# Kernel tuning notes

Hardware: AMD Instinct MI355X
Metric: run time of the kernel (lower is better)

The kernel has to match this reference:

```python
import jax, jax.numpy as jnp
import numpy as np

N = 50000      # nodes of type 'student'
E = 625000     # edges per relation
H = 128        # hidden_channels
C = 6          # num_classes
F_IN = 3       # hardcoded num_features in the module


def setup_inputs() -> dict:
    key = jax.random.key(0)
    ks = jax.random.split(key, 32)
    s = 0.05
    d = {}
    d["x_student"] = jax.random.normal(ks[0], (N, F_IN), dtype=jnp.float32)
    d["ei_friend"] = jax.random.randint(ks[1], (2, E), 0, N)
    d["ei_study"] = jax.random.randint(ks[2], (2, E), 0, N)
    # embedding Linear(3 -> H)
    d["emb_w"] = jax.random.normal(ks[3], (F_IN, H), dtype=jnp.float32) * s
    d["emb_b"] = jnp.zeros((H,), jnp.float32)
    # per-layer, per-edge-type RGCNConv params: relation-0 weight, root weight, bias
    i = 4
    for l in range(2):
        for e in ("f", "s"):
            d[f"w_rel_{l}_{e}"] = jax.random.normal(ks[i], (H, H), dtype=jnp.float32) * s; i += 1
            d[f"w_root_{l}_{e}"] = jax.random.normal(ks[i], (H, H), dtype=jnp.float32) * s; i += 1
            d[f"b_{l}_{e}"] = jnp.zeros((H,), jnp.float32)
    # output Linear(H -> C)
    d["out_w"] = jax.random.normal(ks[i], (H, C), dtype=jnp.float32) * s
    d["out_b"] = jnp.zeros((C,), jnp.float32)
    return d


def _rgcn_conv(h, ei, w_rel, w_root, b):
    # PyG RGCNConv with edge_type==0 everywhere: mean-aggregate src features at dst,
    # project by relation-0 weight, add root transform and bias.
    src, dst = ei[0], ei[1]
    msg = h[src]                                             # [E, H] gather
    agg = jax.ops.segment_sum(msg, dst, num_segments=N)      # [N, H]
    deg = jax.ops.segment_sum(jnp.ones((ei.shape[1],), h.dtype), dst, num_segments=N)
    agg = agg / jnp.maximum(deg, 1.0)[:, None]               # mean aggr (0 for isolated nodes)
    return agg @ w_rel + h @ w_root + b


def reference(x_student, ei_friend, ei_study, emb_w, emb_b,
              w_rel_0_f, w_root_0_f, b_0_f, w_rel_0_s, w_root_0_s, b_0_s,
              w_rel_1_f, w_root_1_f, b_1_f, w_rel_1_s, w_root_1_s, b_1_s,
              out_w, out_b):
    h = jax.nn.relu(x_student @ emb_w + emb_b)
    # layer 0: sum over the two relations, divide by valid_edge_count=2, relu (dropout eval=no-op)
    acc = _rgcn_conv(h, ei_friend, w_rel_0_f, w_root_0_f, b_0_f) \
        + _rgcn_conv(h, ei_study, w_rel_0_s, w_root_0_s, b_0_s)
    h = jax.nn.relu(acc / 2.0)
    # layer 1 (last): no relu/dropout
    acc = _rgcn_conv(h, ei_friend, w_rel_1_f, w_root_1_f, b_1_f) \
        + _rgcn_conv(h, ei_study, w_rel_1_s, w_root_1_s, b_1_s)
    h = acc / 2.0
    return h @ out_w + out_b
```

## Files before the change

kernel.cpp:

```cpp
#include <hip/hip_runtime.h>

#define NN 50000
#define NE 625000
#define HD 128
#define CAP 40
#define ZROW NN

typedef __attribute__((ext_vector_type(8))) short short8;
typedef __attribute__((ext_vector_type(4))) float f32x4;
typedef __attribute__((ext_vector_type(4))) unsigned uint4v;

__device__ __forceinline__ unsigned short f2bf(float f) {
    unsigned u = __builtin_bit_cast(unsigned, f);
    u += 0x7FFFu + ((u >> 16) & 1u);
    return (unsigned short)(u >> 16);
}
__device__ __forceinline__ float bflo(unsigned v) { unsigned u = v << 16; return __builtin_bit_cast(float, u); }
__device__ __forceinline__ float bfhi(unsigned v) { unsigned u = v & 0xFFFF0000u; return __builtin_bit_cast(float, u); }

__device__ __forceinline__ void extract8(uint4v u, int j0, int cnt, unsigned* out) {
    unsigned raw[8];
    raw[0] = u.x & 0xFFFFu; raw[1] = u.x >> 16;
    raw[2] = u.y & 0xFFFFu; raw[3] = u.y >> 16;
    raw[4] = u.z & 0xFFFFu; raw[5] = u.z >> 16;
    raw[6] = u.w & 0xFFFFu; raw[7] = u.w >> 16;
    #pragma unroll
    for (int j = 0; j < 8; ++j) out[j] = (j0 + j < cnt) ? raw[j] : ZROW;
}

__global__ __launch_bounds__(256) void k_prep(
    const float* __restrict__ x, const float* __restrict__ w,
    const float* __restrict__ b, unsigned* __restrict__ h0, unsigned* __restrict__ h1,
    const int* __restrict__ ei_f, const int* __restrict__ ei_s,
    int* __restrict__ degF, int* __restrict__ degS,
    unsigned short* __restrict__ bktF, unsigned short* __restrict__ bktS,
    const float* __restrict__ wrf0, const float* __restrict__ wtf0, const float* __restrict__ bf0,
    const float* __restrict__ wrs0, const float* __restrict__ wts0, const float* __restrict__ bs0,
    const float* __restrict__ wrf1, const float* __restrict__ wtf1, const float* __restrict__ bf1,
    const float* __restrict__ wrs1, const float* __restrict__ wts1, const float* __restrict__ bs1,
    unsigned short* __restrict__ Wt, float* __restrict__ bcat)
{
    int bid = blockIdx.x, t = threadIdx.x;
    if (bid < 12500) {
        int i = bid * 256 + t;
        int n = i >> 6, c = (i & 63) * 2;
        float x0 = x[n*3+0], x1 = x[n*3+1], x2 = x[n*3+2];
        float v0 = fmaf(x0, w[c],   fmaf(x1, w[HD+c],   fmaf(x2, w[2*HD+c],   b[c])));
        float v1 = fmaf(x0, w[c+1], fmaf(x1, w[HD+c+1], fmaf(x2, w[2*HD+c+1], b[c+1])));
        v0 = fmaxf(v0, 0.f); v1 = fmaxf(v1, 0.f);
        h0[i] = (unsigned)f2bf(v0) | ((unsigned)f2bf(v1) << 16);
    } else if (bid == 12500) {
        if (t < 64)       h0[(long)ZROW*64 + t] = 0u;
        else if (t < 128) h1[(long)ZROW*64 + (t - 64)] = 0u;
    } else if (bid < 12885) {
        int i = (bid - 12501) * 256 + t;
        int ln = i / 384, k = i - ln * 384;
        int l = ln >> 7, n = ln & 127;
        const float* wrf = l ? wrf1 : wrf0;
        const float* wrs = l ? wrs1 : wrs0;
        const float* wtf = l ? wtf1 : wtf0;
        const float* wts = l ? wts1 : wts0;
        float v;
        if (k < 128)      v = wrf[k*HD + n];
        else if (k < 256) v = wrs[(k-128)*HD + n];
        else              v = wtf[(k-256)*HD + n] + wts[(k-256)*HD + n];
        Wt[(long)ln*384 + k] = f2bf(0.5f * v);
        if (i < 256) {
            int ll = i >> 7, cc = i & 127;
            const float* bfp = ll ? bf1 : bf0;
            const float* bsp = ll ? bs1 : bs0;
            bcat[i] = 0.5f * (bfp[cc] + bsp[cc]);
        }
    } else {
        int bq = bid - 12885;
        int rel = bq >= 1960;
        int bqq = bq - rel * 1960;
        int cls = bqq & 7;
        int chunk = bqq >> 3;
        const int* ei; int* deg; unsigned short* bkt;
        if (rel == 0) { ei = ei_f; deg = degF; bkt = bktF; }
        else          { ei = ei_s; deg = degS; bkt = bktS; }
        const int lo = cls * 6250, hi = lo + 6250;
        int e0 = chunk * 2560 + t;
        #pragma unroll
        for (int i = 0; i < 10; ++i) {
            int e = e0 + i * 256;
            if (e >= NE) continue;
            int d = ei[NE + e];
            if (d >= lo && d < hi) {
                int s = ei[e];
                int pos = atomicAdd(&deg[d], 1);
                if (pos < CAP) bkt[d*CAP + pos] = (unsigned short)s;
            }
        }
    }
}

__global__ __launch_bounds__(256) void k_spmm(
    const unsigned* __restrict__ h,
    const int* __restrict__ degF, const int* __restrict__ degS,
    const unsigned short* __restrict__ bktF, const unsigned short* __restrict__ bktS,
    unsigned* __restrict__ aggF, unsigned* __restrict__ aggS)
{
    int w = threadIdx.x >> 6, lane = threadIdx.x & 63;
    int n = blockIdx.x * 4 + w;
    int dF = degF[n], dS = degS[n];
    int cF = min(dF, CAP), cS = min(dS, CAP);
    const unsigned short* rowF = bktF + n*CAP;
    const unsigned short* rowS = bktS + n*CAP;
    uint4v uF0 = *(const uint4v*)(rowF);
    uint4v uF1 = *(const uint4v*)(rowF + 8);
    uint4v uS0 = *(const uint4v*)(rowS);
    uint4v uS1 = *(const uint4v*)(rowS + 8);
    unsigned iF[16], iS[16];
    extract8(uF0, 0, cF, iF); extract8(uF1, 8, cF, iF + 8);
    extract8(uS0, 0, cS, iS); extract8(uS1, 8, cS, iS + 8);
    unsigned vF[16], vS[16];
    #pragma unroll
    for (int j = 0; j < 16; ++j) vF[j] = h[iF[j]*64u + lane];
    #pragma unroll
    for (int j = 0; j < 16; ++j) vS[j] = h[iS[j]*64u + lane];
    float aF0 = 0.f, aF1 = 0.f, aS0 = 0.f, aS1 = 0.f;
    #pragma unroll
    for (int j = 0; j < 16; ++j) { aF0 += bflo(vF[j]); aF1 += bfhi(vF[j]); }
    #pragma unroll
    for (int j = 0; j < 16; ++j) { aS0 += bflo(vS[j]); aS1 += bfhi(vS[j]); }
    for (int j = 16; j < cF; j += 8) {
        uint4v u = *(const uint4v*)(rowF + j);
        unsigned ii[8];
        extract8(u, j, cF, ii);
        unsigned vv[8];
        #pragma unroll
        for (int q = 0; q < 8; ++q) vv[q] = h[ii[q]*64u + lane];
        #pragma unroll
        for (int q = 0; q < 8; ++q) { aF0 += bflo(vv[q]); aF1 += bfhi(vv[q]); }
    }
    for (int j = 16; j < cS; j += 8) {
        uint4v u = *(const uint4v*)(rowS + j);
        unsigned ii[8];
        extract8(u, j, cS, ii);
        unsigned vv[8];
        #pragma unroll
        for (int q = 0; q < 8; ++q) vv[q] = h[ii[q]*64u + lane];
        #pragma unroll
        for (int q = 0; q < 8; ++q) { aS0 += bflo(vv[q]); aS1 += bfhi(vv[q]); }
    }
    float invF = 1.f / fmaxf((float)dF, 1.f);
    float invS = 1.f / fmaxf((float)dS, 1.f);
    aggF[n*64 + lane] = (unsigned)f2bf(aF0*invF) | ((unsigned)f2bf(aF1*invF) << 16);
    aggS[n*64 + lane] = (unsigned)f2bf(aS0*invS) | ((unsigned)f2bf(aS1*invS) << 16);
}

__global__ __launch_bounds__(256) void k_gemm(
    const unsigned short* __restrict__ A0, const unsigned short* __restrict__ A1,
    const unsigned short* __restrict__ A2,
    const unsigned short* __restrict__ Wt, const float* __restrict__ bias,
    unsigned short* __restrict__ outH, int mode,
    const float* __restrict__ ow, const float* __restrict__ ob,
    float* __restrict__ out6)
{
    __shared__ unsigned short Bs[16 * 64 * 8];
    const int t = threadIdx.x;
    const int wv = t >> 6, lane = t & 63;
    const int m16 = lane & 15, quad = lane >> 4;
    const int row0 = blockIdx.x * 128 + wv * 32;
    f32x4 acc[2][8];
    #pragma unroll
    for (int mt = 0; mt < 2; ++mt)
        #pragma unroll
        for (int nt = 0; nt < 8; ++nt) acc[mt][nt] = (f32x4){0.f,0.f,0.f,0.f};

    for (int ch = 0; ch < 6; ++ch) {
        const int k0 = ch * 64;
        const unsigned short* src; int kofs;
        if (ch < 2)      { src = A0; kofs = k0; }
        else if (ch < 4) { src = A1; kofs = k0 - 128; }
        else             { src = A2; kofs = k0 - 256; }
        __syncthreads();
        #pragma unroll
        for (int i = 0; i < 4; ++i) {
            int flat = i * 256 + t;
            int fb = flat >> 6, ln = flat & 63;
            int nt = fb >> 1, kc2 = fb & 1;
            int mm = ln & 15, qq = ln >> 4;
            short8 v = *(const short8*)(Wt + (long)(nt*16 + mm)*384 + k0 + kc2*32 + qq*8);
            *(short8*)(Bs + flat*8) = v;
        }
        short8 a[2][2];
        #pragma unroll
        for (int mt = 0; mt < 2; ++mt) {
            int r = row0 + mt*16 + m16;
            #pragma unroll
            for (int kc2 = 0; kc2 < 2; ++kc2) {
                if (r < NN) a[mt][kc2] = *(const short8*)(src + (long)r*HD + kofs + kc2*32 + quad*8);
                else        a[mt][kc2] = short8{0,0,0,0,0,0,0,0};
            }
        }
        __syncthreads();
        #pragma unroll
        for (int kc2 = 0; kc2 < 2; ++kc2)
            #pragma unroll
            for (int nt = 0; nt < 8; ++nt) {
                short8 bfr = *(const short8*)(Bs + ((nt*2 + kc2)*64 + lane)*8);
                acc[0][nt] = __builtin_amdgcn_mfma_f32_16x16x32_bf16(a[0][kc2], bfr, acc[0][nt], 0, 0, 0);
                acc[1][nt] = __builtin_amdgcn_mfma_f32_16x16x32_bf16(a[1][kc2], bfr, acc[1][nt], 0, 0, 0);
            }
    }

    float bs[8];
    #pragma unroll
    for (int nt = 0; nt < 8; ++nt) bs[nt] = bias[nt*16 + m16];

    if (mode == 0) {
        #pragma unroll
        for (int mt = 0; mt < 2; ++mt)
            #pragma unroll
            for (int reg = 0; reg < 4; ++reg) {
                int r = row0 + mt*16 + quad*4 + reg;
                if (r >= NN) continue;
                #pragma unroll
                for (int nt = 0; nt < 8; ++nt) {
                    float v = fmaxf(acc[mt][nt][reg] + bs[nt], 0.f);
                    outH[(long)r*HD + nt*16 + m16] = f2bf(v);
                }
            }
    } else {
        float owr[8][6];
        #pragma unroll
        for (int nt = 0; nt < 8; ++nt) {
            int c = nt*16 + m16;
            #pragma unroll
            for (int j = 0; j < 6; ++j) owr[nt][j] = ow[c*6 + j];
        }
        #pragma unroll
        for (int mt = 0; mt < 2; ++mt)
            #pragma unroll
            for (int reg = 0; reg < 4; ++reg) {
                int r = row0 + mt*16 + quad*4 + reg;
                float tj[6] = {0,0,0,0,0,0};
                #pragma unroll
                for (int nt = 0; nt < 8; ++nt) {
                    float hv = acc[mt][nt][reg] + bs[nt];
                    #pragma unroll
                    for (int j = 0; j < 6; ++j) tj[j] = fmaf(hv, owr[nt][j], tj[j]);
                }
                #pragma unroll
                for (int mask = 1; mask < 16; mask <<= 1)
                    #pragma unroll
                    for (int j = 0; j < 6; ++j) tj[j] += __shfl_xor(tj[j], mask, 64);
                if (m16 == 0 && r < NN) {
                    #pragma unroll
                    for (int j = 0; j < 6; ++j) out6[(long)r*6 + j] = tj[j] + ob[j];
                }
            }
    }
}

extern "C" void kernel_launch(void* const* d_in, const int* in_sizes, int n_in,
                              void* d_out, int out_size, void* d_ws, size_t ws_size,
                              hipStream_t stream)
{
    const float* x     = (const float*)d_in[0];
    const int*   ei_f  = (const int*)d_in[1];
    const int*   ei_s  = (const int*)d_in[2];
    const float* emb_w = (const float*)d_in[3];
    const float* emb_b = (const float*)d_in[4];
    const float* wr0f  = (const float*)d_in[5];
    const float* wt0f  = (const float*)d_in[6];
    const float* b0f   = (const float*)d_in[7];
    const float* wr0s  = (const float*)d_in[8];
    const float* wt0s  = (const float*)d_in[9];
    const float* b0s   = (const float*)d_in[10];
    const float* wr1f  = (const float*)d_in[11];
    const float* wt1f  = (const float*)d_in[12];
    const float* b1f   = (const float*)d_in[13];
    const float* wr1s  = (const float*)d_in[14];
    const float* wt1s  = (const float*)d_in[15];
    const float* b1s   = (const float*)d_in[16];
    const float* out_w = (const float*)d_in[17];
    const float* out_b = (const float*)d_in[18];
    float* out = (float*)d_out;

    char* ws = (char*)d_ws;
    size_t off = 0;
    auto alloc = [&](size_t bytes) { char* p = ws + off; off += (bytes + 255) & ~255ULL; return p; };
    unsigned* h0   = (unsigned*)alloc((size_t)(NN+1)*64*4);
    unsigned* h1   = (unsigned*)alloc((size_t)(NN+1)*64*4);
    unsigned* aggF = (unsigned*)alloc((size_t)NN*64*4);
    unsigned* aggS = (unsigned*)alloc((size_t)NN*64*4);
    int*   degF = (int*)alloc((size_t)NN*4);
    int*   degS = (int*)alloc((size_t)NN*4);
    unsigned short* bktF = (unsigned short*)alloc((size_t)NN*CAP*2);
    unsigned short* bktS = (unsigned short*)alloc((size_t)NN*CAP*2);
    unsigned short* Wt = (unsigned short*)alloc((size_t)2*128*384*2);
    float* bcat = (float*)alloc((size_t)2*HD*4);

    hipMemsetAsync(degF, 0, NN*4, stream);
    hipMemsetAsync(degS, 0, NN*4, stream);

    k_prep<<<16805, 256, 0, stream>>>(x, emb_w, emb_b, h0, h1,
                                      ei_f, ei_s, degF, degS, bktF, bktS,
                                      wr0f, wt0f, b0f, wr0s, wt0s, b0s,
                                      wr1f, wt1f, b1f, wr1s, wt1s, b1s,
                                      Wt, bcat);
    k_spmm<<<NN/4, 256, 0, stream>>>(h0, degF, degS, bktF, bktS, aggF, aggS);
    k_gemm<<<(NN + 127)/128, 256, 0, stream>>>((const unsigned short*)aggF, (const unsigned short*)aggS,
                                               (const unsigned short*)h0, Wt, bcat,
                                               (unsigned short*)h1, 0, out_w, out_b, out);
    k_spmm<<<NN/4, 256, 0, stream>>>(h1, degF, degS, bktF, bktS, aggF, aggS);
    k_gemm<<<(NN + 127)/128, 256, 0, stream>>>((const unsigned short*)aggF, (const unsigned short*)aggS,
                                               (const unsigned short*)h1, Wt + 128*384, bcat + HD,
                                               (unsigned short*)h1, 1, out_w, out_b, out);
}
```

Baseline: 279.5 us.

## Build per-node edge buckets in LDS per destination range, drop global atomics

Replaces the global-atomic bucketing of edges with blocks that each own a range of 768 destination nodes, scan the whole edge list with vector loads, bucket into shared memory with LDS atomics, then copy buckets and degrees out coalesced. This removes the degree memsets and contended global atomics. In exchange every block rereads the full edge list, so total edge traffic grows many times and only 132 blocks perform it.

```diff
diff --git a/kernel.cpp b/kernel.cpp
--- a/kernel.cpp
+++ b/kernel.cpp
@@ -5,6 +5,8 @@
 #define HD 128
 #define CAP 40
 #define ZROW NN
+#define DPB 768
+#define NBKT 66
 
 typedef __attribute__((ext_vector_type(8))) short short8;
 typedef __attribute__((ext_vector_type(4))) float f32x4;
@@ -14,6 +16,9 @@
     unsigned u = __builtin_bit_cast(unsigned, f);
     u += 0x7FFFu + ((u >> 16) & 1u);
     return (unsigned short)(u >> 16);
+}
+__device__ __forceinline__ unsigned pack2(float lo, float hi) {
+    return (unsigned)f2bf(lo) | ((unsigned)f2bf(hi) << 16);
 }
 __device__ __forceinline__ float bflo(unsigned v) { unsigned u = v << 16; return __builtin_bit_cast(float, u); }
 __device__ __forceinline__ float bfhi(unsigned v) { unsigned u = v & 0xFFFF0000u; return __builtin_bit_cast(float, u); }
@@ -40,20 +45,48 @@
     const float* __restrict__ wrs1, const float* __restrict__ wts1, const float* __restrict__ bs1,
     unsigned short* __restrict__ Wt, float* __restrict__ bcat)
 {
+    __shared__ unsigned short lbkt[DPB * CAP];
+    __shared__ int ldeg[DPB];
     int bid = blockIdx.x, t = threadIdx.x;
-    if (bid < 12500) {
-        int i = bid * 256 + t;
+    if (bid < 2 * NBKT) {
+        int rel = bid & 1, idx = bid >> 1;
+        const int* ei = rel ? ei_s : ei_f;
+        int* deg = rel ? degS : degF;
+        unsigned short* bkt = rel ? bktS : bktF;
+        const unsigned lo = idx * DPB;
+        const int nd = min(DPB, NN - (int)lo);
+        for (int j = t; j < DPB; j += 256) ldeg[j] = 0;
+        __syncthreads();
+        const uint4v* dstv = (const uint4v*)(ei + NE);
+        const uint4v* srcv = (const uint4v*)(ei);
+        for (int i = t; i < NE / 4; i += 256) {
+            uint4v d4 = dstv[i];
+            uint4v s4 = srcv[i];
+            unsigned dd;
+            dd = d4.x - lo; if (dd < (unsigned)DPB) { int p = atomicAdd(&ldeg[dd], 1); if (p < CAP) lbkt[dd*CAP + p] = (unsigned short)s4.x; }
+            dd = d4.y - lo; if (dd < (unsigned)DPB) { int p = atomicAdd(&ldeg[dd], 1); if (p < CAP) lbkt[dd*CAP + p] = (unsigned short)s4.y; }
+            dd = d4.z - lo; if (dd < (unsigned)DPB) { int p = atomicAdd(&ldeg[dd], 1); if (p < CAP) lbkt[dd*CAP + p] = (unsigned short)s4.z; }
+            dd = d4.w - lo; if (dd < (unsigned)DPB) { int p = atomicAdd(&ldeg[dd], 1); if (p < CAP) lbkt[dd*CAP + p] = (unsigned short)s4.w; }
+        }
+        __syncthreads();
+        for (int j = t; j < nd; j += 256) deg[lo + j] = ldeg[j];
+        const int ndw = nd * (CAP / 2);
+        unsigned* gb = (unsigned*)(bkt + (long)lo * CAP);
+        const unsigned* lb = (const unsigned*)lbkt;
+        for (int j = t; j < ndw; j += 256) gb[j] = lb[j];
+    } else if (bid < 12632) {
+        int i = (bid - 132) * 256 + t;
         int n = i >> 6, c = (i & 63) * 2;
         float x0 = x[n*3+0], x1 = x[n*3+1], x2 = x[n*3+2];
         float v0 = fmaf(x0, w[c],   fmaf(x1, w[HD+c],   fmaf(x2, w[2*HD+c],   b[c])));
         float v1 = fmaf(x0, w[c+1], fmaf(x1, w[HD+c+1], fmaf(x2, w[2*HD+c+1], b[c+1])));
         v0 = fmaxf(v0, 0.f); v1 = fmaxf(v1, 0.f);
-        h0[i] = (unsigned)f2bf(v0) | ((unsigned)f2bf(v1) << 16);
-    } else if (bid == 12500) {
+        h0[i] = pack2(v0, v1);
+    } else if (bid == 12632) {
         if (t < 64)       h0[(long)ZROW*64 + t] = 0u;
         else if (t < 128) h1[(long)ZROW*64 + (t - 64)] = 0u;
-    } else if (bid < 12885) {
-        int i = (bid - 12501) * 256 + t;
+    } else {
+        int i = (bid - 12633) * 256 + t;
         int ln = i / 384, k = i - ln * 384;
         int l = ln >> 7, n = ln & 127;
         const float* wrf = l ? wrf1 : wrf0;
@@ -71,28 +104,6 @@
             const float* bsp = ll ? bs1 : bs0;
             bcat[i] = 0.5f * (bfp[cc] + bsp[cc]);
         }
-    } else {
-        int bq = bid - 12885;
-        int rel = bq >= 1960;
-        int bqq = bq - rel * 1960;
-        int cls = bqq & 7;
-        int chunk = bqq >> 3;
-        const int* ei; int* deg; unsigned short* bkt;
-        if (rel == 0) { ei = ei_f; deg = degF; bkt = bktF; }
-        else          { ei = ei_s; deg = degS; bkt = bktS; }
-        const int lo = cls * 6250, hi = lo + 6250;
-        int e0 = chunk * 2560 + t;
-        #pragma unroll
-        for (int i = 0; i < 10; ++i) {
-            int e = e0 + i * 256;
-            if (e >= NE) continue;
-            int d = ei[NE + e];
-            if (d >= lo && d < hi) {
-                int s = ei[e];
-                int pos = atomicAdd(&deg[d], 1);
-                if (pos < CAP) bkt[d*CAP + pos] = (unsigned short)s;
-            }
-        }
     }
 }
 
@@ -106,8 +117,8 @@
     int n = blockIdx.x * 4 + w;
     int dF = degF[n], dS = degS[n];
     int cF = min(dF, CAP), cS = min(dS, CAP);
-    const unsigned short* rowF = bktF + n*CAP;
-    const unsigned short* rowS = bktS + n*CAP;
+    const unsigned short* rowF = bktF + (long)n*CAP;
+    const unsigned short* rowS = bktS + (long)n*CAP;
     uint4v uF0 = *(const uint4v*)(rowF);
     uint4v uF1 = *(const uint4v*)(rowF + 8);
     uint4v uS0 = *(const uint4v*)(rowS);
@@ -147,8 +158,8 @@
     }
     float invF = 1.f / fmaxf((float)dF, 1.f);
     float invS = 1.f / fmaxf((float)dS, 1.f);
-    aggF[n*64 + lane] = (unsigned)f2bf(aF0*invF) | ((unsigned)f2bf(aF1*invF) << 16);
-    aggS[n*64 + lane] = (unsigned)f2bf(aS0*invS) | ((unsigned)f2bf(aS1*invS) << 16);
+    aggF[n*64 + lane] = pack2(aF0*invF, aF1*invF);
+    aggS[n*64 + lane] = pack2(aS0*invS, aS1*invS);
 }
 
 __global__ __launch_bounds__(256) void k_gemm(
@@ -290,15 +301,12 @@
     unsigned* aggS = (unsigned*)alloc((size_t)NN*64*4);
     int*   degF = (int*)alloc((size_t)NN*4);
     int*   degS = (int*)alloc((size_t)NN*4);
-    unsigned short* bktF = (unsigned short*)alloc((size_t)NN*CAP*2);
-    unsigned short* bktS = (unsigned short*)alloc((size_t)NN*CAP*2);
+    unsigned short* bktF = (unsigned short*)alloc((size_t)(NBKT*DPB)*CAP*2);
+    unsigned short* bktS = (unsigned short*)alloc((size_t)(NBKT*DPB)*CAP*2);
     unsigned short* Wt = (unsigned short*)alloc((size_t)2*128*384*2);
     float* bcat = (float*)alloc((size_t)2*HD*4);
 
-    hipMemsetAsync(degF, 0, NN*4, stream);
-    hipMemsetAsync(degS, 0, NN*4, stream);
-
-    k_prep<<<16805, 256, 0, stream>>>(x, emb_w, emb_b, h0, h1,
+    k_prep<<<13017, 256, 0, stream>>>(x, emb_w, emb_b, h0, h1,
                                       ei_f, ei_s, degF, degS, bktF, bktS,
                                       wr0f, wt0f, b0f, wr0s, wt0s, b0s,
                                       wr1f, wt1f, b1f, wr1s, wt1s, b1s,
```

New measurement: 484.3 us. +73.3%, slower.
